# Kernel tuning notes

Hardware: AMD Instinct MI355X
Metric: run time of the kernel (lower is better)

The kernel has to match this reference:

```python
import jax, jax.numpy as jnp
import numpy as np

NUM_HEADS = 12
SCALE = 1.0 / np.sqrt(768 // NUM_HEADS)  # 0.125


def setup_inputs() -> dict:
    key = jax.random.key(0)
    k1, k2, k3, k4, k5 = jax.random.split(key, 5)
    B, N, C = 4, 2048, 768
    x = jax.random.normal(k1, (B, N, C), dtype=jnp.float32)
    qkv_w = jax.random.normal(k2, (3 * C, C), dtype=jnp.float32) * 0.02
    qkv_b = jax.random.normal(k3, (3 * C,), dtype=jnp.float32) * 0.02
    proj_w = jax.random.normal(k4, (C, C), dtype=jnp.float32) * 0.02
    proj_b = jax.random.normal(k5, (C,), dtype=jnp.float32) * 0.02
    return {"x": x, "qkv_w": qkv_w, "qkv_b": qkv_b, "proj_w": proj_w, "proj_b": proj_b}


def reference(x, qkv_w, qkv_b, proj_w, proj_b):
    B, N, C = x.shape
    H = NUM_HEADS
    Dh = C // H
    # qkv projection (torch Linear: x @ W^T + b)
    qkv = x @ qkv_w.T + qkv_b                      # [B, N, 3C]
    qkv = qkv.reshape(B, N, 3, H, Dh).transpose(2, 0, 3, 1, 4)  # [3, B, H, N, Dh]
    q, k, v = qkv[0], qkv[1], qkv[2]
    q = q * SCALE
    attn = jnp.einsum("bhnd,bhmd->bhnm", q, k)     # [B, H, N, N]
    attn = jax.nn.softmax(attn, axis=-1)
    out = jnp.einsum("bhnm,bhmd->bhnd", attn, v)   # [B, H, N, Dh]
    out = out.transpose(0, 2, 1, 3).reshape(B, N, C)
    out = out @ proj_w.T + proj_b
    return out
```

## Files before the change

### kernel.cpp

```cpp
#include <hip/hip_runtime.h>
#include <math.h>

typedef __attribute__((ext_vector_type(8))) short short8;
typedef __attribute__((ext_vector_type(4))) float f32x4;
typedef __attribute__((ext_vector_type(16))) float f32x16;

namespace {

constexpr int B  = 4;
constexpr int N  = 2048;
constexpr int C  = 768;
constexpr int H  = 12;
constexpr int Dh = 64;
constexpr int M  = B * N;
constexpr int C3 = 3 * C;

constexpr float QSCALE = 0.125f * 1.4426950408889634f;

__device__ inline unsigned short f2bf(float x) {
  unsigned int u = __float_as_uint(x);
  return (unsigned short)((u + 0x7fffu + ((u >> 16) & 1u)) >> 16);
}

__device__ inline unsigned cvt_pk_bf16(float lo, float hi) {
  unsigned r;
  asm("v_cvt_pk_bf16_f32 %0, %1, %2" : "=v"(r) : "v"(lo), "v"(hi));
  return r;
}

__device__ inline void gload_lds16(const void* g, void* lds) {
  __builtin_amdgcn_global_load_lds(
      (const __attribute__((address_space(1))) void*)g,
      (__attribute__((address_space(3))) void*)lds, 16, 0, 0);
}

__device__ inline float max3f(float a, float b, float c) {
  return fmaxf(fmaxf(a, b), c);
}

__global__ __launch_bounds__(256) void cvt_all3(
    const float* __restrict__ x, const float* __restrict__ qw,
    const float* __restrict__ pw, unsigned short* __restrict__ xbf,
    unsigned short* __restrict__ wqkv, unsigned short* __restrict__ wproj) {
  constexpr int n1 = M * C / 4, n2 = C3 * C / 4, n3 = C * C / 4;
  constexpr int tot = n1 + n2 + n3;
  for (int i = blockIdx.x * 256 + threadIdx.x; i < tot; i += gridDim.x * 256) {
    const float4* s; unsigned short* d; int j;
    if (i < n1)            { s = (const float4*)x;  d = xbf;   j = i; }
    else if (i < n1 + n2)  { s = (const float4*)qw; d = wqkv;  j = i - n1; }
    else                   { s = (const float4*)pw; d = wproj; j = i - n1 - n2; }
    float4 v = s[j];
    ushort4 o;
    o.x = f2bf(v.x); o.y = f2bf(v.y); o.z = f2bf(v.z); o.w = f2bf(v.w);
    reinterpret_cast<ushort4*>(d)[j] = o;
  }
}

template <bool QKV_EPI>
__global__ __launch_bounds__(256, 2) void gemm_mfma_bt(
    const unsigned short* __restrict__ A, const unsigned short* __restrict__ Bw,
    const float* __restrict__ bias, void* __restrict__ outp, int Nd, int K) {
  __shared__ alignas(16) unsigned short lA[128 * 64];
  __shared__ alignas(16) unsigned short lB[128 * 64];
  const int t = threadIdx.x, wave = t >> 6, lane = t & 63;
  const int bm = blockIdx.x * 128, bn = blockIdx.y * 128;
  const int wr = (wave >> 1) * 64, wc = (wave & 1) * 64;

  f32x4 acc[4][4];
#pragma unroll
  for (int i = 0; i < 4; ++i)
#pragma unroll
    for (int j = 0; j < 4; ++j) acc[i][j] = (f32x4){0.f, 0.f, 0.f, 0.f};

  const int srow = lane >> 3;
  const int scol = ((lane & 7) ^ srow) * 8;
  const int rb0  = wave * 32;

  for (int k0 = 0; k0 < K; k0 += 64) {
#pragma unroll
    for (int i = 0; i < 4; ++i) {
      const int rb = rb0 + i * 8;
      const unsigned short* ga = A  + (size_t)(bm + rb + srow) * K + k0 + scol;
      const unsigned short* gb = Bw + (size_t)(bn + rb + srow) * K + k0 + scol;
      gload_lds16(ga, (char*)lA + rb * 128);
      gload_lds16(gb, (char*)lB + rb * 128);
    }
    __syncthreads();

#pragma unroll
    for (int kc = 0; kc < 2; ++kc) {
      short8 af[4], bfr[4];
#pragma unroll
      for (int mt = 0; mt < 4; ++mt) {
        const int row = wr + mt * 16 + (lane & 15);
        const int q = (row * 128 + kc * 64 + (lane >> 4) * 16) ^ ((row & 7) << 4);
        af[mt] = *reinterpret_cast<const short8*>((const char*)lA + q);
      }
#pragma unroll
      for (int nt = 0; nt < 4; ++nt) {
        const int row = wc + nt * 16 + (lane & 15);
        const int q = (row * 128 + kc * 64 + (lane >> 4) * 16) ^ ((row & 7) << 4);
        bfr[nt] = *reinterpret_cast<const short8*>((const char*)lB + q);
      }
#pragma unroll
      for (int mt = 0; mt < 4; ++mt)
#pragma unroll
        for (int nt = 0; nt < 4; ++nt)
          acc[mt][nt] = __builtin_amdgcn_mfma_f32_16x16x32_bf16(
              af[mt], bfr[nt], acc[mt][nt], 0, 0, 0);
    }
    __syncthreads();
  }

  const int r0 = (lane >> 4) * 4;
  const int cl = lane & 15;
#pragma unroll
  for (int nt = 0; nt < 4; ++nt) {
    const int col = bn + wc + nt * 16 + cl;
    const float bs = bias[col];
    const float sc = (QKV_EPI && col < C) ? QSCALE : 1.0f;
#pragma unroll
    for (int mt = 0; mt < 4; ++mt) {
#pragma unroll
      for (int r = 0; r < 4; ++r) {
        const size_t row = bm + wr + mt * 16 + r0 + r;
        const float v = acc[mt][nt][r] + bs;
        if (QKV_EPI)
          ((unsigned short*)outp)[row * Nd + col] = f2bf(v * sc);
        else
          ((float*)outp)[row * Nd + col] = v;
      }
    }
  }
}

__global__ __launch_bounds__(256) void vt_prepass(
    const unsigned short* __restrict__ qkvbf, unsigned short* __restrict__ vt) {
  const int bh = blockIdx.x, b = bh / H, h = bh % H;
  const int nt = blockIdx.y;
  __shared__ unsigned short tile[64][72];
  const int t = threadIdx.x;
  const int r = t >> 2, ch = (t & 3) * 16;

  const unsigned short* src =
      qkvbf + (size_t)(b * N + nt * 64 + r) * C3 + 2 * C + h * Dh + ch;
  *reinterpret_cast<int4*>(&tile[r][ch])     = *reinterpret_cast<const int4*>(src);
  *reinterpret_cast<int4*>(&tile[r][ch + 8]) = *reinterpret_cast<const int4*>(src + 8);
  __syncthreads();

  alignas(16) unsigned short vals[16];
#pragma unroll
  for (int i = 0; i < 16; ++i) vals[i] = tile[ch + i][r];
  unsigned short* dst = vt + ((size_t)bh * Dh + r) * N + nt * 64 + ch;
  *reinterpret_cast<int4*>(dst)     = *reinterpret_cast<int4*>(&vals[0]);
  *reinterpret_cast<int4*>(dst + 8) = *reinterpret_cast<int4*>(&vals[8]);
}

__global__ __launch_bounds__(256) void attn_mfma32(
    const unsigned short* __restrict__ qkvbf,
    const unsigned short* __restrict__ vt,
    unsigned short* __restrict__ ctx) {
  const int bh = blockIdx.x, b = bh / H, h = bh % H;
  const int qt = blockIdx.y;
  const int t = threadIdx.x;
  const int wave = t >> 6, lane = t & 63;
  const int ql = lane & 31;
  const int hi = lane >> 5;
  const int q0 = qt * 128 + wave * 32;

  __shared__ alignas(16) char lds[3][16384];

  short8 qf[4];
  {
    const unsigned short* qrow =
        qkvbf + (size_t)(b * N + q0 + ql) * C3 + h * Dh + 8 * hi;
#pragma unroll
    for (int s = 0; s < 4; ++s) {
      int4 v = *reinterpret_cast<const int4*>(qrow + 16 * s);
      qf[s] = *reinterpret_cast<short8*>(&v);
    }
  }

  f32x16 ot0, ot1;
#pragma unroll
  for (int r = 0; r < 16; ++r) { ot0[r] = 0.f; ot1[r] = 0.f; }
  float mrun = -INFINITY, lrun = 0.f;

  const int rl = lane >> 3;
  const int cs = ((lane & 7) ^ rl) * 8;
  const size_t kgbase = (size_t)(b * N) * C3 + C + h * Dh;
  const unsigned short* kstg =
      qkvbf + kgbase + (size_t)(wave * 16 + rl) * C3 + cs;
  const unsigned short* vstg =
      vt + ((size_t)bh * Dh + wave * 16 + rl) * N + cs;

  auto stage = [&](int j) {
    char* bufc = lds[j % 3];
    const unsigned short* kp = kstg + (size_t)(j * 64) * C3;
    const unsigned short* vp = vstg + j * 64;
    char* kd = bufc + (wave * 16) * 128;
    char* vd = bufc + 8192 + (wave * 16) * 128;
    gload_lds16(kp,          kd);
    gload_lds16(kp + 8 * C3, kd + 8 * 128);
    gload_lds16(vp,          vd);
    gload_lds16(vp + 8 * N,  vd + 8 * 128);
  };

  constexpr int NT = N / 64;

  auto kaddr = [&](int row, int s) {
    return (row * 128 + 32 * s + 16 * hi) ^ ((row & 7) << 4);
  };

  stage(0);
  stage(1);

  for (int kt = 0; kt < NT; ++kt) {
    if (kt < NT - 1) asm volatile("s_waitcnt vmcnt(4)" ::: "memory");
    else             asm volatile("s_waitcnt vmcnt(0)" ::: "memory");
    __builtin_amdgcn_s_barrier();
    __builtin_amdgcn_sched_barrier(0);

    if (kt + 2 < NT) stage(kt + 2);

    const char* bufc = lds[kt % 3];

    f32x16 s0, s1;
#pragma unroll
    for (int r = 0; r < 16; ++r) { s0[r] = 0.f; s1[r] = 0.f; }
    __builtin_amdgcn_s_setprio(1);
#pragma unroll
    for (int s = 0; s < 4; ++s) {
      short8 k0 = *reinterpret_cast<const short8*>(bufc + kaddr(ql, s));
      short8 k1 = *reinterpret_cast<const short8*>(bufc + kaddr(32 + ql, s));
      s0 = __builtin_amdgcn_mfma_f32_32x32x16_bf16(k0, qf[s], s0, 0, 0, 0);
      s1 = __builtin_amdgcn_mfma_f32_32x32x16_bf16(k1, qf[s], s1, 0, 0, 0);
    }
    __builtin_amdgcn_s_setprio(0);

    short8 vf[8];
    const char* bufv = bufc + 8192;
#pragma unroll
    for (int s = 0; s < 4; ++s) {
      vf[2 * s]     = *reinterpret_cast<const short8*>(bufv + kaddr(ql, s));
      vf[2 * s + 1] = *reinterpret_cast<const short8*>(bufv + kaddr(32 + ql, s));
    }

    float t0 = max3f(s0[0], s0[1], s0[2]);
    float t1 = max3f(s0[3], s0[4], s0[5]);
    float t2 = max3f(s0[6], s0[7], s0[8]);
    float t3 = max3f(s0[9], s0[10], s0[11]);
    float t4 = max3f(s0[12], s0[13], s0[14]);
    float t5 = max3f(s0[15], s1[0], s1[1]);
    float t6 = max3f(s1[2], s1[3], s1[4]);
    float t7 = max3f(s1[5], s1[6], s1[7]);
    float t8 = max3f(s1[8], s1[9], s1[10]);
    float t9 = max3f(s1[11], s1[12], s1[13]);
    float ta = fmaxf(s1[14], s1[15]);
    t0 = max3f(t0, t1, t2);
    t3 = max3f(t3, t4, t5);
    t6 = max3f(t6, t7, t8);
    t9 = max3f(t9, ta, t0);
    const float mx = max3f(t3, t6, t9);
    if (!__all(mx <= mrun + 8.f)) {
      const float nm = fmaxf(mrun, fmaxf(mx, __shfl_xor(mx, 32)));
      const float corr = __builtin_amdgcn_exp2f(mrun - nm);
      lrun *= corr;
#pragma unroll
      for (int r = 0; r < 16; ++r) {
        const int qr = (r & 3) + 8 * (r >> 2) + 4 * hi;
        const float cr = __shfl(corr, qr);
        ot0[r] *= cr; ot1[r] *= cr;
      }
      mrun = nm;
    }

    short8 pf0, pf1, pf2, pf3;
    auto mkfrag = [&](const f32x16& sh, short8& fA, short8& fB) {
      float e[16];
#pragma unroll
      for (int r = 0; r < 16; ++r) e[r] = __builtin_amdgcn_exp2f(sh[r] - mrun);
      lrun += (((e[0] + e[1]) + (e[2] + e[3])) + ((e[4] + e[5]) + (e[6] + e[7]))) +
              (((e[8] + e[9]) + (e[10] + e[11])) + ((e[12] + e[13]) + (e[14] + e[15])));
      unsigned w[8];
#pragma unroll
      for (int tt = 0; tt < 4; ++tt) {
        w[2 * tt]     = cvt_pk_bf16(e[4 * tt], e[4 * tt + 1]);
        w[2 * tt + 1] = cvt_pk_bf16(e[4 * tt + 2], e[4 * tt + 3]);
      }
      unsigned a0 = w[0], a1 = w[1], b0 = w[2], b1 = w[3];
      asm("v_permlane32_swap_b32 %0, %1" : "+v"(a0), "+v"(b0));
      asm("v_permlane32_swap_b32 %0, %1" : "+v"(a1), "+v"(b1));
      int4 p0; p0.x = a0; p0.y = a1; p0.z = b0; p0.w = b1;
      fA = *reinterpret_cast<short8*>(&p0);
      unsigned c0 = w[4], c1 = w[5], d0 = w[6], d1 = w[7];
      asm("v_permlane32_swap_b32 %0, %1" : "+v"(c0), "+v"(d0));
      asm("v_permlane32_swap_b32 %0, %1" : "+v"(c1), "+v"(d1));
      int4 p1; p1.x = c0; p1.y = c1; p1.z = d0; p1.w = d1;
      fB = *reinterpret_cast<short8*>(&p1);
    };
    mkfrag(s0, pf0, pf1);
    mkfrag(s1, pf2, pf3);

    __builtin_amdgcn_s_setprio(1);
    ot0 = __builtin_amdgcn_mfma_f32_32x32x16_bf16(pf0, vf[0], ot0, 0, 0, 0);
    ot1 = __builtin_amdgcn_mfma_f32_32x32x16_bf16(pf0, vf[1], ot1, 0, 0, 0);
    ot0 = __builtin_amdgcn_mfma_f32_32x32x16_bf16(pf1, vf[2], ot0, 0, 0, 0);
    ot1 = __builtin_amdgcn_mfma_f32_32x32x16_bf16(pf1, vf[3], ot1, 0, 0, 0);
    ot0 = __builtin_amdgcn_mfma_f32_32x32x16_bf16(pf2, vf[4], ot0, 0, 0, 0);
    ot1 = __builtin_amdgcn_mfma_f32_32x32x16_bf16(pf2, vf[5], ot1, 0, 0, 0);
    ot0 = __builtin_amdgcn_mfma_f32_32x32x16_bf16(pf3, vf[6], ot0, 0, 0, 0);
    ot1 = __builtin_amdgcn_mfma_f32_32x32x16_bf16(pf3, vf[7], ot1, 0, 0, 0);
    __builtin_amdgcn_s_setprio(0);
  }

  lrun += __shfl_xor(lrun, 32);
  const float inv = 1.f / lrun;
#pragma unroll
  for (int r = 0; r < 16; ++r) {
    const int qr = (r & 3) + 8 * (r >> 2) + 4 * hi;
    const float ir = __shfl(inv, qr);
    unsigned short* orow = ctx + (size_t)(b * N + q0 + qr) * C + h * Dh;
    orow[ql]      = f2bf(ot0[r] * ir);
    orow[32 + ql] = f2bf(ot1[r] * ir);
  }
}

}

extern "C" void kernel_launch(void* const* d_in, const int* in_sizes, int n_in,
                              void* d_out, int out_size, void* d_ws, size_t ws_size,
                              hipStream_t stream) {
  const float* x      = (const float*)d_in[0];
  const float* qkv_w  = (const float*)d_in[1];
  const float* qkv_b  = (const float*)d_in[2];
  const float* proj_w = (const float*)d_in[3];
  const float* proj_b = (const float*)d_in[4];
  float* out = (float*)d_out;

  unsigned short* qkvbf = (unsigned short*)d_ws;
  unsigned short* ctx   = qkvbf + (size_t)M * C3;
  unsigned short* vt    = ctx + (size_t)M * C;
  unsigned short* xbf   = vt + (size_t)M * C;
  unsigned short* wqkv  = xbf + (size_t)M * C;
  unsigned short* wproj = wqkv + (size_t)C3 * C;

  cvt_all3<<<2048, 256, 0, stream>>>(x, qkv_w, proj_w, xbf, wqkv, wproj);

  gemm_mfma_bt<true>
      <<<dim3(M / 128, C3 / 128), 256, 0, stream>>>(xbf, wqkv, qkv_b, qkvbf, C3, C);
  vt_prepass<<<dim3(B * H, N / 64), 256, 0, stream>>>(qkvbf, vt);
  attn_mfma32<<<dim3(B * H, N / 128), 256, 0, stream>>>(qkvbf, vt, ctx);
  gemm_mfma_bt<false>
      <<<dim3(M / 128, C / 128), 256, 0, stream>>>(ctx, wproj, proj_b, out, C, C);
}
```

Before: 149.0 us.

## Give each attention wave two 32-row query tiles and halve waves per block

The attention kernel now runs 2 waves per block instead of 4, and each wave handles 64 query rows as two 32-row sub-tiles. This reuses each K and V fragment read from LDS across twice as many MFMAs. K/V staging goes from triple to double buffering, with wave 0 loading K and wave 1 loading V, and a __syncthreads at the end of each iteration replaces the vmcnt-based waits. The intent is to cut LDS read traffic per MFMA, at the cost of higher register pressure (four output accumulators), fewer waves to hide latency, and a less overlapped prefetch since each tile is loaded only one iteration ahead.

Result: no change. 148.4 us (-0.4%).

```diff
diff --git a/kernel.cpp b/kernel.cpp
--- a/kernel.cpp
+++ b/kernel.cpp
@@ -156,7 +156,7 @@
   *reinterpret_cast<int4*>(dst + 8) = *reinterpret_cast<int4*>(&vals[8]);
 }
 
-__global__ __launch_bounds__(256) void attn_mfma32(
+__global__ __launch_bounds__(128, 2) void attn_mfma32(
     const unsigned short* __restrict__ qkvbf,
     const unsigned short* __restrict__ vt,
     unsigned short* __restrict__ ctx) {
@@ -166,44 +166,48 @@
   const int wave = t >> 6, lane = t & 63;
   const int ql = lane & 31;
   const int hi = lane >> 5;
-  const int q0 = qt * 128 + wave * 32;
-
-  __shared__ alignas(16) char lds[3][16384];
-
-  short8 qf[4];
+  const int q0 = qt * 128 + wave * 64;
+
+  __shared__ alignas(16) char lds[2][16384];
+
+  short8 qfa[4], qfb[4];
   {
-    const unsigned short* qrow =
+    const unsigned short* qa =
         qkvbf + (size_t)(b * N + q0 + ql) * C3 + h * Dh + 8 * hi;
+    const unsigned short* qb = qa + (size_t)32 * C3;
 #pragma unroll
     for (int s = 0; s < 4; ++s) {
-      int4 v = *reinterpret_cast<const int4*>(qrow + 16 * s);
-      qf[s] = *reinterpret_cast<short8*>(&v);
-    }
-  }
-
-  f32x16 ot0, ot1;
-#pragma unroll
-  for (int r = 0; r < 16; ++r) { ot0[r] = 0.f; ot1[r] = 0.f; }
-  float mrun = -INFINITY, lrun = 0.f;
+      int4 va = *reinterpret_cast<const int4*>(qa + 16 * s);
+      int4 vb = *reinterpret_cast<const int4*>(qb + 16 * s);
+      qfa[s] = *reinterpret_cast<short8*>(&va);
+      qfb[s] = *reinterpret_cast<short8*>(&vb);
+    }
+  }
+
+  f32x16 zz;
+#pragma unroll
+  for (int r = 0; r < 16; ++r) zz[r] = 0.f;
+  f32x16 oa0 = zz, oa1 = zz, ob0 = zz, ob1 = zz;
+  float mra = -INFINITY, mrb = -INFINITY, la = 0.f, lb = 0.f;
 
   const int rl = lane >> 3;
-  const int cs = ((lane & 7) ^ rl) * 8;
-  const size_t kgbase = (size_t)(b * N) * C3 + C + h * Dh;
+  const int cse = ((lane & 7) ^ rl) * 8;
   const unsigned short* kstg =
-      qkvbf + kgbase + (size_t)(wave * 16 + rl) * C3 + cs;
-  const unsigned short* vstg =
-      vt + ((size_t)bh * Dh + wave * 16 + rl) * N + cs;
-
-  auto stage = [&](int j) {
-    char* bufc = lds[j % 3];
-    const unsigned short* kp = kstg + (size_t)(j * 64) * C3;
-    const unsigned short* vp = vstg + j * 64;
-    char* kd = bufc + (wave * 16) * 128;
-    char* vd = bufc + 8192 + (wave * 16) * 128;
-    gload_lds16(kp,          kd);
-    gload_lds16(kp + 8 * C3, kd + 8 * 128);
-    gload_lds16(vp,          vd);
-    gload_lds16(vp + 8 * N,  vd + 8 * 128);
+      qkvbf + (size_t)(b * N + rl) * C3 + C + h * Dh + cse;
+  const unsigned short* vstg = vt + ((size_t)bh * Dh + rl) * N + cse;
+
+  auto stage = [&](int kt, char* buf) {
+    if (wave == 0) {
+      const unsigned short* kp = kstg + (size_t)(kt * 64) * C3;
+#pragma unroll
+      for (int j = 0; j < 8; ++j)
+        gload_lds16(kp + (size_t)(j * 8) * C3, buf + j * 1024);
+    } else {
+      const unsigned short* vp = vstg + kt * 64;
+#pragma unroll
+      for (int j = 0; j < 8; ++j)
+        gload_lds16(vp + (size_t)(j * 8) * N, buf + 8192 + j * 1024);
+    }
   };
 
   constexpr int NT = N / 64;
@@ -212,75 +216,87 @@
     return (row * 128 + 32 * s + 16 * hi) ^ ((row & 7) << 4);
   };
 
-  stage(0);
-  stage(1);
+  stage(0, lds[0]);
+  __syncthreads();
 
   for (int kt = 0; kt < NT; ++kt) {
-    if (kt < NT - 1) asm volatile("s_waitcnt vmcnt(4)" ::: "memory");
-    else             asm volatile("s_waitcnt vmcnt(0)" ::: "memory");
-    __builtin_amdgcn_s_barrier();
-    __builtin_amdgcn_sched_barrier(0);
-
-    if (kt + 2 < NT) stage(kt + 2);
-
-    const char* bufc = lds[kt % 3];
-
-    f32x16 s0, s1;
-#pragma unroll
-    for (int r = 0; r < 16; ++r) { s0[r] = 0.f; s1[r] = 0.f; }
+    const char* bufc = lds[kt & 1];
+    if (kt + 1 < NT) stage(kt + 1, lds[(kt + 1) & 1]);
+
+    short8 k0[4], k1[4];
+#pragma unroll
+    for (int s = 0; s < 4; ++s) {
+      k0[s] = *reinterpret_cast<const short8*>(bufc + kaddr(ql, s));
+      k1[s] = *reinterpret_cast<const short8*>(bufc + kaddr(32 + ql, s));
+    }
+
+    f32x16 sa0, sa1, sb0, sb1;
     __builtin_amdgcn_s_setprio(1);
+    sa0 = __builtin_amdgcn_mfma_f32_32x32x16_bf16(k0[0], qfa[0], zz, 0, 0, 0);
+    sa1 = __builtin_amdgcn_mfma_f32_32x32x16_bf16(k1[0], qfa[0], zz, 0, 0, 0);
+    sb0 = __builtin_amdgcn_mfma_f32_32x32x16_bf16(k0[0], qfb[0], zz, 0, 0, 0);
+    sb1 = __builtin_amdgcn_mfma_f32_32x32x16_bf16(k1[0], qfb[0], zz, 0, 0, 0);
+#pragma unroll
+    for (int s = 1; s < 4; ++s) {
+      sa0 = __builtin_amdgcn_mfma_f32_32x32x16_bf16(k0[s], qfa[s], sa0, 0, 0, 0);
+      sa1 = __builtin_amdgcn_mfma_f32_32x32x16_bf16(k1[s], qfa[s], sa1, 0, 0, 0);
+      sb0 = __builtin_amdgcn_mfma_f32_32x32x16_bf16(k0[s], qfb[s], sb0, 0, 0, 0);
+      sb1 = __builtin_amdgcn_mfma_f32_32x32x16_bf16(k1[s], qfb[s], sb1, 0, 0, 0);
+    }
+    __builtin_amdgcn_s_setprio(0);
+
+    short8 vfr[8];
+    const char* bufv = bufc + 8192;
 #pragma unroll
     for (int s = 0; s < 4; ++s) {
-      short8 k0 = *reinterpret_cast<const short8*>(bufc + kaddr(ql, s));
-      short8 k1 = *reinterpret_cast<const short8*>(bufc + kaddr(32 + ql, s));
-      s0 = __builtin_amdgcn_mfma_f32_32x32x16_bf16(k0, qf[s], s0, 0, 0, 0);
-      s1 = __builtin_amdgcn_mfma_f32_32x32x16_bf16(k1, qf[s], s1, 0, 0, 0);
-    }
-    __builtin_amdgcn_s_setprio(0);
-
-    short8 vf[8];
-    const char* bufv = bufc + 8192;
-#pragma unroll
-    for (int s = 0; s < 4; ++s) {
-      vf[2 * s]     = *reinterpret_cast<const short8*>(bufv + kaddr(ql, s));
-      vf[2 * s + 1] = *reinterpret_cast<const short8*>(bufv + kaddr(32 + ql, s));
-    }
-
-    float t0 = max3f(s0[0], s0[1], s0[2]);
-    float t1 = max3f(s0[3], s0[4], s0[5]);
-    float t2 = max3f(s0[6], s0[7], s0[8]);
-    float t3 = max3f(s0[9], s0[10], s0[11]);
-    float t4 = max3f(s0[12], s0[13], s0[14]);
-    float t5 = max3f(s0[15], s1[0], s1[1]);
-    float t6 = max3f(s1[2], s1[3], s1[4]);
-    float t7 = max3f(s1[5], s1[6], s1[7]);
-    float t8 = max3f(s1[8], s1[9], s1[10]);
-    float t9 = max3f(s1[11], s1[12], s1[13]);
-    float ta = fmaxf(s1[14], s1[15]);
-    t0 = max3f(t0, t1, t2);
-    t3 = max3f(t3, t4, t5);
-    t6 = max3f(t6, t7, t8);
-    t9 = max3f(t9, ta, t0);
-    const float mx = max3f(t3, t6, t9);
-    if (!__all(mx <= mrun + 8.f)) {
-      const float nm = fmaxf(mrun, fmaxf(mx, __shfl_xor(mx, 32)));
-      const float corr = __builtin_amdgcn_exp2f(mrun - nm);
-      lrun *= corr;
+      vfr[2 * s]     = *reinterpret_cast<const short8*>(bufv + kaddr(ql, s));
+      vfr[2 * s + 1] = *reinterpret_cast<const short8*>(bufv + kaddr(32 + ql, s));
+    }
+
+    auto rmax = [&](const f32x16& x, const f32x16& y) {
+      float t0 = max3f(x[0], x[1], x[2]);
+      float t1 = max3f(x[3], x[4], x[5]);
+      float t2 = max3f(x[6], x[7], x[8]);
+      float t3 = max3f(x[9], x[10], x[11]);
+      float t4 = max3f(x[12], x[13], x[14]);
+      float t5 = max3f(x[15], y[0], y[1]);
+      float t6 = max3f(y[2], y[3], y[4]);
+      float t7 = max3f(y[5], y[6], y[7]);
+      float t8 = max3f(y[8], y[9], y[10]);
+      float t9 = max3f(y[11], y[12], y[13]);
+      float ta = fmaxf(y[14], y[15]);
+      t0 = max3f(t0, t1, t2);
+      t3 = max3f(t3, t4, t5);
+      t6 = max3f(t6, t7, t8);
+      t9 = max3f(t9, ta, t0);
+      return max3f(t3, t6, t9);
+    };
+    const float mxa = rmax(sa0, sa1);
+    const float mxb = rmax(sb0, sb1);
+    const bool fast = (mxa <= mra + 8.f) && (mxb <= mrb + 8.f);
+    if (!__all(fast)) {
+      const float nma = fmaxf(mra, fmaxf(mxa, __shfl_xor(mxa, 32)));
+      const float nmb = fmaxf(mrb, fmaxf(mxb, __shfl_xor(mxb, 32)));
+      const float ca = __builtin_amdgcn_exp2f(mra - nma);
+      const float cb = __builtin_amdgcn_exp2f(mrb - nmb);
+      la *= ca; lb *= cb;
 #pragma unroll
       for (int r = 0; r < 16; ++r) {
         const int qr = (r & 3) + 8 * (r >> 2) + 4 * hi;
-        const float cr = __shfl(corr, qr);
-        ot0[r] *= cr; ot1[r] *= cr;
-      }
-      mrun = nm;
-    }
-
-    short8 pf0, pf1, pf2, pf3;
-    auto mkfrag = [&](const f32x16& sh, short8& fA, short8& fB) {
+        const float cra = __shfl(ca, qr);
+        const float crb = __shfl(cb, qr);
+        oa0[r] *= cra; oa1[r] *= cra;
+        ob0[r] *= crb; ob1[r] *= crb;
+      }
+      mra = nma; mrb = nmb;
+    }
+
+    auto mkfrag = [&](const f32x16& sh, float mr, float& lacc,
+                      short8& fA, short8& fB) {
       float e[16];
 #pragma unroll
-      for (int r = 0; r < 16; ++r) e[r] = __builtin_amdgcn_exp2f(sh[r] - mrun);
-      lrun += (((e[0] + e[1]) + (e[2] + e[3])) + ((e[4] + e[5]) + (e[6] + e[7]))) +
+      for (int r = 0; r < 16; ++r) e[r] = __builtin_amdgcn_exp2f(sh[r] - mr);
+      lacc += (((e[0] + e[1]) + (e[2] + e[3])) + ((e[4] + e[5]) + (e[6] + e[7]))) +
               (((e[8] + e[9]) + (e[10] + e[11])) + ((e[12] + e[13]) + (e[14] + e[15])));
       unsigned w[8];
 #pragma unroll
@@ -299,30 +315,49 @@
       int4 p1; p1.x = c0; p1.y = c1; p1.z = d0; p1.w = d1;
       fB = *reinterpret_cast<short8*>(&p1);
     };
-    mkfrag(s0, pf0, pf1);
-    mkfrag(s1, pf2, pf3);
+    short8 pa0, pa1, pa2, pa3, pb0, pb1, pb2, pb3;
+    mkfrag(sa0, mra, la, pa0, pa1);
+    mkfrag(sa1, mra, la, pa2, pa3);
+    mkfrag(sb0, mrb, lb, pb0, pb1);
+    mkfrag(sb1, mrb, lb, pb2, pb3);
 
     __builtin_amdgcn_s_setprio(1);
-    ot0 = __builtin_amdgcn_mfma_f32_32x32x16_bf16(pf0, vf[0], ot0, 0, 0, 0);
-    ot1 = __builtin_amdgcn_mfma_f32_32x32x16_bf16(pf0, vf[1], ot1, 0, 0, 0);
-    ot0 = __builtin_amdgcn_mfma_f32_32x32x16_bf16(pf1, vf[2], ot0, 0, 0, 0);
-    ot1 = __builtin_amdgcn_mfma_f32_32x32x16_bf16(pf1, vf[3], ot1, 0, 0, 0);
-    ot0 = __builtin_amdgcn_mfma_f32_32x32x16_bf16(pf2, vf[4], ot0, 0, 0, 0);
-    ot1 = __builtin_amdgcn_mfma_f32_32x32x16_bf16(pf2, vf[5], ot1, 0, 0, 0);
-    ot0 = __builtin_amdgcn_mfma_f32_32x32x16_bf16(pf3, vf[6], ot0, 0, 0, 0);
-    ot1 = __builtin_amdgcn_mfma_f32_32x32x16_bf16(pf3, vf[7], ot1, 0, 0, 0);
+    oa0 = __builtin_amdgcn_mfma_f32_32x32x16_bf16(pa0, vfr[0], oa0, 0, 0, 0);
+    oa1 = __builtin_amdgcn_mfma_f32_32x32x16_bf16(pa0, vfr[1], oa1, 0, 0, 0);
+    ob0 = __builtin_amdgcn_mfma_f32_32x32x16_bf16(pb0, vfr[0], ob0, 0, 0, 0);
+    ob1 = __builtin_amdgcn_mfma_f32_32x32x16_bf16(pb0, vfr[1], ob1, 0, 0, 0);
+    oa0 = __builtin_amdgcn_mfma_f32_32x32x16_bf16(pa1, vfr[2], oa0, 0, 0, 0);
+    oa1 = __builtin_amdgcn_mfma_f32_32x32x16_bf16(pa1, vfr[3], oa1, 0, 0, 0);
+    ob0 = __builtin_amdgcn_mfma_f32_32x32x16_bf16(pb1, vfr[2], ob0, 0, 0, 0);
+    ob1 = __builtin_amdgcn_mfma_f32_32x32x16_bf16(pb1, vfr[3], ob1, 0, 0, 0);
+    oa0 = __builtin_amdgcn_mfma_f32_32x32x16_bf16(pa2, vfr[4], oa0, 0, 0, 0);
+    oa1 = __builtin_amdgcn_mfma_f32_32x32x16_bf16(pa2, vfr[5], oa1, 0, 0, 0);
+    ob0 = __builtin_amdgcn_mfma_f32_32x32x16_bf16(pb2, vfr[4], ob0, 0, 0, 0);
+    ob1 = __builtin_amdgcn_mfma_f32_32x32x16_bf16(pb2, vfr[5], ob1, 0, 0, 0);
+    oa0 = __builtin_amdgcn_mfma_f32_32x32x16_bf16(pa3, vfr[6], oa0, 0, 0, 0);
+    oa1 = __builtin_amdgcn_mfma_f32_32x32x16_bf16(pa3, vfr[7], oa1, 0, 0, 0);
+    ob0 = __builtin_amdgcn_mfma_f32_32x32x16_bf16(pb3, vfr[6], ob0, 0, 0, 0);
+    ob1 = __builtin_amdgcn_mfma_f32_32x32x16_bf16(pb3, vfr[7], ob1, 0, 0, 0);
     __builtin_amdgcn_s_setprio(0);
-  }
-
-  lrun += __shfl_xor(lrun, 32);
-  const float inv = 1.f / lrun;
+
+    __syncthreads();
+  }
+
+  la += __shfl_xor(la, 32);
+  lb += __shfl_xor(lb, 32);
+  const float inva = 1.f / la;
+  const float invb = 1.f / lb;
 #pragma unroll
   for (int r = 0; r < 16; ++r) {
     const int qr = (r & 3) + 8 * (r >> 2) + 4 * hi;
-    const float ir = __shfl(inv, qr);
-    unsigned short* orow = ctx + (size_t)(b * N + q0 + qr) * C + h * Dh;
-    orow[ql]      = f2bf(ot0[r] * ir);
-    orow[32 + ql] = f2bf(ot1[r] * ir);
+    const float ira = __shfl(inva, qr);
+    const float irb = __shfl(invb, qr);
+    unsigned short* rowa = ctx + (size_t)(b * N + q0 + qr) * C + h * Dh;
+    unsigned short* rowb = rowa + (size_t)32 * C;
+    rowa[ql]      = f2bf(oa0[r] * ira);
+    rowa[32 + ql] = f2bf(oa1[r] * ira);
+    rowb[ql]      = f2bf(ob0[r] * irb);
+    rowb[32 + ql] = f2bf(ob1[r] * irb);
   }
 }
 
@@ -350,7 +385,7 @@
   gemm_mfma_bt<true>
       <<<dim3(M / 128, C3 / 128), 256, 0, stream>>>(xbf, wqkv, qkv_b, qkvbf, C3, C);
   vt_prepass<<<dim3(B * H, N / 64), 256, 0, stream>>>(qkvbf, vt);
-  attn_mfma32<<<dim3(B * H, N / 128), 256, 0, stream>>>(qkvbf, vt, ctx);
+  attn_mfma32<<<dim3(B * H, N / 128), 128, 0, stream>>>(qkvbf, vt, ctx);
   gemm_mfma_bt<false>
       <<<dim3(M / 128, C / 128), 256, 0, stream>>>(ctx, wproj, proj_b, out, C, C);
 }
```

## Fuse V transpose into QKV GEMM epilogue; compute softmax row sums via MFMA

Applied to the files above, without the earlier changes.

The QKV GEMM epilogue now writes V straight into a transposed per-head layout, so the separate vt_prepass kernel and its extra read and write of V are gone. The attention kernel accumulates softmax denominators with an extra MFMA against a ones vector, replacing the per-lane exp-sum and the final shuffle. It also drops the 3-deep async LDS pipeline with vmcnt waits for a 2-buffer scheme with a full __syncthreads each iteration. That loses load/compute overlap and adds barrier cost, plus four extra MFMAs per tile.

Measured after the change: 144.8 us. 2.8% less time.

```diff
diff --git a/kernel.cpp b/kernel.cpp
--- a/kernel.cpp
+++ b/kernel.cpp
@@ -59,7 +59,8 @@
 template <bool QKV_EPI>
 __global__ __launch_bounds__(256, 2) void gemm_mfma_bt(
     const unsigned short* __restrict__ A, const unsigned short* __restrict__ Bw,
-    const float* __restrict__ bias, void* __restrict__ outp, int Nd, int K) {
+    const float* __restrict__ bias, void* __restrict__ outp,
+    unsigned short* __restrict__ vtp, int Nd, int K) {
   __shared__ alignas(16) unsigned short lA[128 * 64];
   __shared__ alignas(16) unsigned short lB[128 * 64];
   const int t = threadIdx.x, wave = t >> 6, lane = t & 63;
@@ -118,42 +119,42 @@
   for (int nt = 0; nt < 4; ++nt) {
     const int col = bn + wc + nt * 16 + cl;
     const float bs = bias[col];
-    const float sc = (QKV_EPI && col < C) ? QSCALE : 1.0f;
-#pragma unroll
-    for (int mt = 0; mt < 4; ++mt) {
-#pragma unroll
-      for (int r = 0; r < 4; ++r) {
-        const size_t row = bm + wr + mt * 16 + r0 + r;
-        const float v = acc[mt][nt][r] + bs;
-        if (QKV_EPI)
-          ((unsigned short*)outp)[row * Nd + col] = f2bf(v * sc);
-        else
-          ((float*)outp)[row * Nd + col] = v;
-      }
-    }
-  }
-}
-
-__global__ __launch_bounds__(256) void vt_prepass(
-    const unsigned short* __restrict__ qkvbf, unsigned short* __restrict__ vt) {
-  const int bh = blockIdx.x, b = bh / H, h = bh % H;
-  const int nt = blockIdx.y;
-  __shared__ unsigned short tile[64][72];
-  const int t = threadIdx.x;
-  const int r = t >> 2, ch = (t & 3) * 16;
-
-  const unsigned short* src =
-      qkvbf + (size_t)(b * N + nt * 64 + r) * C3 + 2 * C + h * Dh + ch;
-  *reinterpret_cast<int4*>(&tile[r][ch])     = *reinterpret_cast<const int4*>(src);
-  *reinterpret_cast<int4*>(&tile[r][ch + 8]) = *reinterpret_cast<const int4*>(src + 8);
-  __syncthreads();
-
-  alignas(16) unsigned short vals[16];
-#pragma unroll
-  for (int i = 0; i < 16; ++i) vals[i] = tile[ch + i][r];
-  unsigned short* dst = vt + ((size_t)bh * Dh + r) * N + nt * 64 + ch;
-  *reinterpret_cast<int4*>(dst)     = *reinterpret_cast<int4*>(&vals[0]);
-  *reinterpret_cast<int4*>(dst + 8) = *reinterpret_cast<int4*>(&vals[8]);
+    if constexpr (QKV_EPI) {
+      if (col < 2 * C) {
+        const float sc = (col < C) ? QSCALE : 1.0f;
+#pragma unroll
+        for (int mt = 0; mt < 4; ++mt)
+#pragma unroll
+          for (int r = 0; r < 4; ++r) {
+            const size_t row = bm + wr + mt * 16 + r0 + r;
+            ((unsigned short*)outp)[row * Nd + col] =
+                f2bf((acc[mt][nt][r] + bs) * sc);
+          }
+      } else {
+        const int hh = (col - 2 * C) >> 6, dd = (col - 2 * C) & 63;
+        const int bb = bm >> 11;
+        unsigned short* vrow = vtp + ((size_t)(bb * H + hh) * Dh + dd) * N;
+#pragma unroll
+        for (int mt = 0; mt < 4; ++mt) {
+          const int n0 = (bm & 2047) + wr + mt * 16 + r0;
+          ushort4 pk;
+          pk.x = f2bf(acc[mt][nt][0] + bs);
+          pk.y = f2bf(acc[mt][nt][1] + bs);
+          pk.z = f2bf(acc[mt][nt][2] + bs);
+          pk.w = f2bf(acc[mt][nt][3] + bs);
+          *reinterpret_cast<ushort4*>(vrow + n0) = pk;
+        }
+      }
+    } else {
+#pragma unroll
+      for (int mt = 0; mt < 4; ++mt)
+#pragma unroll
+        for (int r = 0; r < 4; ++r) {
+          const size_t row = bm + wr + mt * 16 + r0 + r;
+          ((float*)outp)[row * Nd + col] = acc[mt][nt][r] + bs;
+        }
+    }
+  }
 }
 
 __global__ __launch_bounds__(256) void attn_mfma32(
@@ -168,7 +169,7 @@
   const int hi = lane >> 5;
   const int q0 = qt * 128 + wave * 32;
 
-  __shared__ alignas(16) char lds[3][16384];
+  __shared__ alignas(16) char lds[2][16384];
 
   short8 qf[4];
   {
@@ -181,10 +182,14 @@
     }
   }
 
-  f32x16 ot0, ot1;
-#pragma unroll
-  for (int r = 0; r < 16; ++r) { ot0[r] = 0.f; ot1[r] = 0.f; }
-  float mrun = -INFINITY, lrun = 0.f;
+  f32x16 ot0, ot1, l_acc;
+#pragma unroll
+  for (int r = 0; r < 16; ++r) { ot0[r] = 0.f; ot1[r] = 0.f; l_acc[r] = 0.f; }
+  float mrun = -INFINITY;
+
+  short8 ones;
+#pragma unroll
+  for (int i = 0; i < 8; ++i) ones[i] = (short)0x3F80;
 
   const int rl = lane >> 3;
   const int cs = ((lane & 7) ^ rl) * 8;
@@ -194,10 +199,9 @@
   const unsigned short* vstg =
       vt + ((size_t)bh * Dh + wave * 16 + rl) * N + cs;
 
-  auto stage = [&](int j) {
-    char* bufc = lds[j % 3];
-    const unsigned short* kp = kstg + (size_t)(j * 64) * C3;
-    const unsigned short* vp = vstg + j * 64;
+  auto stage = [&](char* bufc, int kt) {
+    const unsigned short* kp = kstg + (size_t)(kt * 64) * C3;
+    const unsigned short* vp = vstg + kt * 64;
     char* kd = bufc + (wave * 16) * 128;
     char* vd = bufc + 8192 + (wave * 16) * 128;
     gload_lds16(kp,          kd);
@@ -212,18 +216,12 @@
     return (row * 128 + 32 * s + 16 * hi) ^ ((row & 7) << 4);
   };
 
-  stage(0);
-  stage(1);
+  stage(lds[0], 0);
+  __syncthreads();
 
   for (int kt = 0; kt < NT; ++kt) {
-    if (kt < NT - 1) asm volatile("s_waitcnt vmcnt(4)" ::: "memory");
-    else             asm volatile("s_waitcnt vmcnt(0)" ::: "memory");
-    __builtin_amdgcn_s_barrier();
-    __builtin_amdgcn_sched_barrier(0);
-
-    if (kt + 2 < NT) stage(kt + 2);
-
-    const char* bufc = lds[kt % 3];
+    const char* bufc = lds[kt & 1];
+    if (kt + 1 < NT) stage(lds[(kt + 1) & 1], kt + 1);
 
     f32x16 s0, s1;
 #pragma unroll
@@ -265,23 +263,19 @@
     if (!__all(mx <= mrun + 8.f)) {
       const float nm = fmaxf(mrun, fmaxf(mx, __shfl_xor(mx, 32)));
       const float corr = __builtin_amdgcn_exp2f(mrun - nm);
-      lrun *= corr;
 #pragma unroll
       for (int r = 0; r < 16; ++r) {
         const int qr = (r & 3) + 8 * (r >> 2) + 4 * hi;
         const float cr = __shfl(corr, qr);
-        ot0[r] *= cr; ot1[r] *= cr;
+        ot0[r] *= cr; ot1[r] *= cr; l_acc[r] *= cr;
       }
       mrun = nm;
     }
 
-    short8 pf0, pf1, pf2, pf3;
     auto mkfrag = [&](const f32x16& sh, short8& fA, short8& fB) {
       float e[16];
 #pragma unroll
       for (int r = 0; r < 16; ++r) e[r] = __builtin_amdgcn_exp2f(sh[r] - mrun);
-      lrun += (((e[0] + e[1]) + (e[2] + e[3])) + ((e[4] + e[5]) + (e[6] + e[7]))) +
-              (((e[8] + e[9]) + (e[10] + e[11])) + ((e[12] + e[13]) + (e[14] + e[15])));
       unsigned w[8];
 #pragma unroll
       for (int tt = 0; tt < 4; ++tt) {
@@ -291,35 +285,40 @@
       unsigned a0 = w[0], a1 = w[1], b0 = w[2], b1 = w[3];
       asm("v_permlane32_swap_b32 %0, %1" : "+v"(a0), "+v"(b0));
       asm("v_permlane32_swap_b32 %0, %1" : "+v"(a1), "+v"(b1));
-      int4 p0; p0.x = a0; p0.y = a1; p0.z = b0; p0.w = b1;
+      int4 p0; p0.x = (int)a0; p0.y = (int)a1; p0.z = (int)b0; p0.w = (int)b1;
       fA = *reinterpret_cast<short8*>(&p0);
       unsigned c0 = w[4], c1 = w[5], d0 = w[6], d1 = w[7];
       asm("v_permlane32_swap_b32 %0, %1" : "+v"(c0), "+v"(d0));
       asm("v_permlane32_swap_b32 %0, %1" : "+v"(c1), "+v"(d1));
-      int4 p1; p1.x = c0; p1.y = c1; p1.z = d0; p1.w = d1;
+      int4 p1; p1.x = (int)c0; p1.y = (int)c1; p1.z = (int)d0; p1.w = (int)d1;
       fB = *reinterpret_cast<short8*>(&p1);
     };
+    short8 pf0, pf1, pf2, pf3;
     mkfrag(s0, pf0, pf1);
     mkfrag(s1, pf2, pf3);
 
     __builtin_amdgcn_s_setprio(1);
+    l_acc = __builtin_amdgcn_mfma_f32_32x32x16_bf16(pf0, ones, l_acc, 0, 0, 0);
     ot0 = __builtin_amdgcn_mfma_f32_32x32x16_bf16(pf0, vf[0], ot0, 0, 0, 0);
     ot1 = __builtin_amdgcn_mfma_f32_32x32x16_bf16(pf0, vf[1], ot1, 0, 0, 0);
+    l_acc = __builtin_amdgcn_mfma_f32_32x32x16_bf16(pf1, ones, l_acc, 0, 0, 0);
     ot0 = __builtin_amdgcn_mfma_f32_32x32x16_bf16(pf1, vf[2], ot0, 0, 0, 0);
     ot1 = __builtin_amdgcn_mfma_f32_32x32x16_bf16(pf1, vf[3], ot1, 0, 0, 0);
+    l_acc = __builtin_amdgcn_mfma_f32_32x32x16_bf16(pf2, ones, l_acc, 0, 0, 0);
     ot0 = __builtin_amdgcn_mfma_f32_32x32x16_bf16(pf2, vf[4], ot0, 0, 0, 0);
     ot1 = __builtin_amdgcn_mfma_f32_32x32x16_bf16(pf2, vf[5], ot1, 0, 0, 0);
+    l_acc = __builtin_amdgcn_mfma_f32_32x32x16_bf16(pf3, ones, l_acc, 0, 0, 0);
     ot0 = __builtin_amdgcn_mfma_f32_32x32x16_bf16(pf3, vf[6], ot0, 0, 0, 0);
     ot1 = __builtin_amdgcn_mfma_f32_32x32x16_bf16(pf3, vf[7], ot1, 0, 0, 0);
     __builtin_amdgcn_s_setprio(0);
-  }
-
-  lrun += __shfl_xor(lrun, 32);
-  const float inv = 1.f / lrun;
+
+    __syncthreads();
+  }
+
 #pragma unroll
   for (int r = 0; r < 16; ++r) {
     const int qr = (r & 3) + 8 * (r >> 2) + 4 * hi;
-    const float ir = __shfl(inv, qr);
+    const float ir = 1.f / l_acc[r];
     unsigned short* orow = ctx + (size_t)(b * N + q0 + qr) * C + h * Dh;
     orow[ql]      = f2bf(ot0[r] * ir);
     orow[32 + ql] = f2bf(ot1[r] * ir);
@@ -347,10 +346,9 @@
 
   cvt_all3<<<2048, 256, 0, stream>>>(x, qkv_w, proj_w, xbf, wqkv, wproj);
 
-  gemm_mfma_bt<true>
-      <<<dim3(M / 128, C3 / 128), 256, 0, stream>>>(xbf, wqkv, qkv_b, qkvbf, C3, C);
-  vt_prepass<<<dim3(B * H, N / 64), 256, 0, stream>>>(qkvbf, vt);
+  gemm_mfma_bt<true><<<dim3(M / 128, C3 / 128), 256, 0, stream>>>(
+      xbf, wqkv, qkv_b, qkvbf, vt, C3, C);
   attn_mfma32<<<dim3(B * H, N / 128), 256, 0, stream>>>(qkvbf, vt, ctx);
-  gemm_mfma_bt<false>
-      <<<dim3(M / 128, C / 128), 256, 0, stream>>>(ctx, wproj, proj_b, out, C, C);
-}
+  gemm_mfma_bt<false><<<dim3(M / 128, C / 128), 256, 0, stream>>>(
+      ctx, wproj, proj_b, out, nullptr, C, C);
+}
```
